# Kernel optimization log

Hardware: AMD Instinct MI355X
Metric: run time of the kernel (lower is better)

Reference implementation:

```python
import jax, jax.numpy as jnp
import numpy as np

H, NH, R = 128, 8, 6
NB = 2                  # geometric interaction blocks
BS, L, K = 16, 64, 16   # graphs, blocks/graph, atoms/block
NBLK = BS * L           # 1024 blocks total
N = NBLK * K            # 16384 atoms
E = 262144              # atom-level edges
EB = 512                # block-level edges per graph
CUTOFF = 8.0


def _mha(x, in_w, in_b, out_w, out_b):
    # torch nn.MultiheadAttention (batch_first, eval / no dropout). x: [B,S,H]
    B_, S, _ = x.shape
    qkv = x @ in_w + in_b                     # [B,S,3H]
    q, k, v = jnp.split(qkv, 3, axis=-1)
    dh = H // NH
    q = q.reshape(B_, S, NH, dh)
    k = k.reshape(B_, S, NH, dh)
    v = v.reshape(B_, S, NH, dh)
    scores = jnp.einsum('bind,bjnd->bnij', q, k) / np.sqrt(dh).astype(np.float32)
    attn = jax.nn.softmax(scores, axis=-1)
    o = jnp.einsum('bnij,bjnd->bind', attn, v).reshape(B_, S, H)
    return o @ out_w + out_b


def _forward(A, atom_positions, B_types, coords, edge_index, block_edges,
             emb_atom, emb_pos, emb_block, rbf_freq,
             inter_w1, inter_b1, inter_w2, inter_b2,
             upd_w1, upd_b1, upd_w2, upd_b2,
             edge_w1, edge_b1, edge_w2, edge_b2,
             attn_in_w, attn_in_b, attn_out_w, attn_out_b,
             ln_g, ln_b, fin_w1, fin_b1, fin_w2, fin_b2, fin_w3, fin_b3):
    block_id = jnp.repeat(jnp.arange(NBLK), K)  # uniform K atoms per block
    # atom embedding + position embedding + broadcast block embedding
    x = emb_atom[A] + emb_pos[atom_positions] + emb_block[B_types][block_id]  # [N,H]

    # ---- GeometricAtomProcessor ----
    i, j = edge_index[0], edge_index[1]
    d = jnp.linalg.norm(coords[i] - coords[j], axis=-1)       # [E]
    u = jnp.clip(d / CUTOFF, 1e-3, None)
    # DimeNet envelope, exponent=5 -> p=6: 1/u + a u^5 + b u^6 + c u^7
    env = 1.0 / u - 28.0 * u**5 + 48.0 * u**6 - 21.0 * u**7
    rbf = env[:, None] * jnp.sin(rbf_freq[None, :] * u[:, None])  # [E,R]

    for b in range(NB):
        ef = jnp.concatenate([x[i], x[j], rbf], axis=-1)       # [E,2H+R] gather
        m = jax.nn.silu(ef @ inter_w1[b] + inter_b1[b]) @ inter_w2[b] + inter_b2[b]
        agg = jax.ops.segment_sum(m, i, num_segments=N)        # index_add_ scatter
        ui = jnp.concatenate([x, agg], axis=-1)
        x = jax.nn.silu(ui @ upd_w1[b] + upd_b1[b]) @ upd_w2[b] + upd_b2[b] + x

    # scatter_mean over block_id (uniform blocks -> reshape mean)
    blocks = x.reshape(NBLK, K, H).mean(axis=1).reshape(BS, L, H)

    # ---- per-graph block-edge attention (batched over graphs) ----
    src, dst = block_edges[..., 0], block_edges[..., 1]        # [BS,EB]
    bidx = jnp.arange(BS)[:, None]
    ef = jnp.concatenate([blocks[bidx, src], blocks[bidx, dst]], axis=-1)  # [BS,EB,2H]
    ef = jax.nn.relu(ef @ edge_w1 + edge_b1) @ edge_w2 + edge_b2
    ea = _mha(ef, attn_in_w, attn_in_b, attn_out_w, attn_out_b)            # [BS,EB,H]
    seg = (src + bidx * L).reshape(-1)
    sums = jax.ops.segment_sum(ea.reshape(-1, H), seg, num_segments=NBLK)
    cnt = jax.ops.segment_sum(jnp.ones((BS * EB,), ea.dtype), seg, num_segments=NBLK)
    blocks = blocks + (sums / jnp.maximum(cnt, 1.0)[:, None]).reshape(BS, L, H)

    # ---- block self-attention + mean pool ----
    att = _mha(blocks, attn_in_w, attn_in_b, attn_out_w, attn_out_b)
    g = att.mean(axis=1)                                       # [BS,H]
    mu = g.mean(-1, keepdims=True)
    var = ((g - mu) ** 2).mean(-1, keepdims=True)
    g = (g - mu) / jnp.sqrt(var + 1e-5) * ln_g + ln_b
    h1 = jax.nn.relu(g @ fin_w1 + fin_b1)
    h2 = jax.nn.relu(h1 @ fin_w2 + fin_b2)
    return (h2 @ fin_w3 + fin_b3).squeeze(-1)                  # [BS]


def setup_inputs() -> dict:
    key = jax.random.key(0)
    ks = jax.random.split(key, 40)
    def nrm(k, shape, s=0.05):
        return jax.random.normal(k, shape, jnp.float32) * s
    inp = {}
    inp['A'] = jax.random.randint(ks[0], (N,), 0, 100)
    inp['atom_positions'] = jax.random.randint(ks[1], (N,), 0, 16)
    inp['B_types'] = jax.random.randint(ks[2], (NBLK,), 0, 1000)
    inp['coords'] = jax.random.uniform(ks[3], (N, 3), jnp.float32, 0.0, 20.0)
    inp['edge_index'] = jax.random.randint(ks[4], (2, E), 0, N)
    inp['block_edges'] = jax.random.randint(ks[5], (BS, EB, 2), 0, L)
    inp['emb_atom'] = nrm(ks[6], (100, H), 0.5)
    inp['emb_pos'] = nrm(ks[7], (16, H), 0.5)
    inp['emb_block'] = nrm(ks[8], (1000, H), 0.5)
    inp['rbf_freq'] = (jnp.arange(1, R + 1, dtype=jnp.float32) * np.pi)
    inp['inter_w1'] = nrm(ks[9], (NB, 2 * H + R, H))
    inp['inter_b1'] = jnp.zeros((NB, H), jnp.float32)
    inp['inter_w2'] = nrm(ks[10], (NB, H, H))
    inp['inter_b2'] = jnp.zeros((NB, H), jnp.float32)
    inp['upd_w1'] = nrm(ks[11], (NB, 2 * H, H))
    inp['upd_b1'] = jnp.zeros((NB, H), jnp.float32)
    inp['upd_w2'] = nrm(ks[12], (NB, H, H))
    inp['upd_b2'] = jnp.zeros((NB, H), jnp.float32)
    inp['edge_w1'] = nrm(ks[13], (2 * H, H))
    inp['edge_b1'] = jnp.zeros((H,), jnp.float32)
    inp['edge_w2'] = nrm(ks[14], (H, H))
    inp['edge_b2'] = jnp.zeros((H,), jnp.float32)
    inp['attn_in_w'] = nrm(ks[15], (H, 3 * H))
    inp['attn_in_b'] = jnp.zeros((3 * H,), jnp.float32)
    inp['attn_out_w'] = nrm(ks[16], (H, H))
    inp['attn_out_b'] = jnp.zeros((H,), jnp.float32)
    inp['ln_g'] = jnp.ones((H,), jnp.float32)
    inp['ln_b'] = jnp.zeros((H,), jnp.float32)
    inp['fin_w1'] = nrm(ks[17], (H, H))
    inp['fin_b1'] = jnp.zeros((H,), jnp.float32)
    inp['fin_w2'] = nrm(ks[18], (H, H))
    inp['fin_b2'] = jnp.zeros((H,), jnp.float32)
    inp['fin_w3'] = nrm(ks[19], (H, 1))
    inp['fin_b3'] = jnp.zeros((1,), jnp.float32)
    return inp


def reference(A, atom_positions, B_types, coords, edge_index, block_edges,
              emb_atom, emb_pos, emb_block, rbf_freq,
              inter_w1, inter_b1, inter_w2, inter_b2,
              upd_w1, upd_b1, upd_w2, upd_b2,
              edge_w1, edge_b1, edge_w2, edge_b2,
              attn_in_w, attn_in_b, attn_out_w, attn_out_b,
              ln_g, ln_b, fin_w1, fin_b1, fin_w2, fin_b2, fin_w3, fin_b3):
    return _forward(A, atom_positions, B_types, coords, edge_index, block_edges,
                    emb_atom, emb_pos, emb_block, rbf_freq,
                    inter_w1, inter_b1, inter_w2, inter_b2,
                    upd_w1, upd_b1, upd_w2, upd_b2,
                    edge_w1, edge_b1, edge_w2, edge_b2,
                    attn_in_w, attn_in_b, attn_out_w, attn_out_b,
                    ln_g, ln_b, fin_w1, fin_b1, fin_w2, fin_b2, fin_w3, fin_b3)
```

## Files before the change

### kernel.cpp

```cpp
#include <hip/hip_runtime.h>
#include <math.h>

#define H 128
#define NHD 8
#define DH 16
#define RB 6
#define NBI 2
#define BSG 16
#define LBLK 64
#define KATOM 16
#define NBLKT 1024
#define NA 16384
#define NE 262144
#define EBE 512

__device__ __forceinline__ float fsilu(float v) {
  return v * __builtin_amdgcn_rcpf(1.0f + __expf(-v));
}

typedef short v4s __attribute__((ext_vector_type(4)));
typedef float f32x4 __attribute__((ext_vector_type(4)));

__device__ __forceinline__ short f2bf(float f) {
  union { float f; unsigned u; } v; v.f = f;
  unsigned r = v.u + 0x7fffu + ((v.u >> 16) & 1u);
  return (short)(r >> 16);
}

__device__ __forceinline__ float bf2f(short s) {
  union { unsigned u; float f; } v;
  v.u = ((unsigned)(unsigned short)s) << 16;
  return v.f;
}

#if defined(__has_builtin)
#if __has_builtin(__builtin_amdgcn_mfma_f32_16x16x16bf16_1k)
#define HAVE_MFMA16_1K 1
#endif
#endif

#ifdef HAVE_MFMA16_1K
__device__ __forceinline__ f32x4 mfma16(v4s a, v4s b, f32x4 c) {
  return __builtin_amdgcn_mfma_f32_16x16x16bf16_1k(a, b, c, 0, 0, 0);
}
#else
typedef short v8s __attribute__((ext_vector_type(8)));
__device__ __forceinline__ f32x4 mfma16(v4s a, v4s b, f32x4 c) {
  v8s a8 = {a[0], a[1], a[2], a[3], 0, 0, 0, 0};
  v8s b8 = {b[0], b[1], b[2], b[3], 0, 0, 0, 0};
  return __builtin_amdgcn_mfma_f32_16x16x32_bf16(a8, b8, c, 0, 0, 0);
}
#endif

__global__ __launch_bounds__(256) void k_hist(
    const int* __restrict__ ei, int* __restrict__ cnt)
{
  int e = blockIdx.x * 256 + threadIdx.x;
  atomicAdd(&cnt[ei[e]], 1);
}

__global__ __launch_bounds__(1024) void k_scan(
    const int* __restrict__ cnt, int* __restrict__ off,
    int* __restrict__ cur, float* __restrict__ cntf)
{
  __shared__ int ps[1024];
  int t = threadIdx.x;
  int base = t * 16;
  int local[16];
  int s = 0;
  #pragma unroll
  for (int k = 0; k < 16; ++k) { local[k] = s; s += cnt[base + k]; }
  ps[t] = s;
  __syncthreads();
  for (int d = 1; d < 1024; d <<= 1) {
    int v = (t >= d) ? ps[t - d] : 0;
    __syncthreads();
    ps[t] += v;
    __syncthreads();
  }
  int offset = (t == 0) ? 0 : ps[t - 1];
  #pragma unroll
  for (int k = 0; k < 16; ++k) {
    int o = offset + local[k];
    off[base + k] = o;
    cur[base + k] = o;
    cntf[base + k] = (float)cnt[base + k];
  }
  if (t == 1023) off[NA] = offset + s;
}

__global__ __launch_bounds__(256) void k_scatter_b(
    const int* __restrict__ ei, const int* __restrict__ ej,
    const float* __restrict__ coords, const float* __restrict__ freq,
    int* __restrict__ cur, int* __restrict__ ej_s, float* __restrict__ rbf_s,
    const int* __restrict__ bedges, int* __restrict__ blist,
    int* __restrict__ boff, float* __restrict__ ind)
{
  __shared__ int hist[64], offs[65], curs[64];
  int t = threadIdx.x;
  if (blockIdx.x < NE / 256) {
    int e = blockIdx.x * 256 + t;
    int i = ei[e], j = ej[e];
    int pos = atomicAdd(&cur[i], 1);
    ej_s[pos] = j;
    float dx = coords[i*3+0] - coords[j*3+0];
    float dy = coords[i*3+1] - coords[j*3+1];
    float dz = coords[i*3+2] - coords[j*3+2];
    float d = sqrtf(dx*dx + dy*dy + dz*dz);
    float u = fmaxf(d * 0.125f, 1e-3f);
    float u2 = u*u, u4 = u2*u2, u5 = u4*u, u6 = u5*u, u7 = u6*u;
    float env = 1.0f/u - 28.0f*u5 + 48.0f*u6 - 21.0f*u7;
    #pragma unroll
    for (int r = 0; r < RB; ++r)
      rbf_s[(size_t)pos*RB + r] = env * __sinf(freq[r] * u);
    return;
  }
  int b = blockIdx.x - NE / 256;
  if (t < 64) hist[t] = 0;
  __syncthreads();
  for (int e = t; e < EBE; e += 256) atomicAdd(&hist[bedges[(b*EBE + e)*2]], 1);
  __syncthreads();
  if (t == 0) {
    offs[0] = 0;
    for (int k = 0; k < 64; ++k) offs[k+1] = offs[k] + hist[k];
  }
  __syncthreads();
  if (t < 64) curs[t] = offs[t];
  __syncthreads();
  for (int e = t; e < EBE; e += 256) {
    int src = bedges[(b*EBE + e)*2];
    int pos = atomicAdd(&curs[src], 1);
    blist[b*EBE + pos] = e;
  }
  if (t < 65) boff[b*65 + t] = offs[t];
  if (t < 64) ind[b*64 + t] = (hist[t] > 0) ? 1.0f : 0.0f;
}

__global__ __launch_bounds__(256) void k_prep(
    const float* __restrict__ W2base, const float* __restrict__ U1base,
    const float* __restrict__ b2base, float* __restrict__ bvecbase,
    short* __restrict__ wt_u1base,
    const float* __restrict__ inter_w1, const float* __restrict__ upd_w2,
    const float* __restrict__ edge_w1, const float* __restrict__ edge_w2,
    const float* __restrict__ attn_in_w,
    short* __restrict__ wt_pq, short* __restrict__ wt_u2,
    short* __restrict__ wt_e1, short* __restrict__ wt_e2,
    short* __restrict__ wt_in)
{
  int bx = blockIdx.x, tid = threadIdx.x;
  if (bx < 128) {
    int k = bx, y = tid >> 7, c = tid & 127;
    const float* W2 = W2base + (size_t)y * H * H;
    const float* U1 = U1base + (size_t)y * 2 * H * H;
    const float* b2 = b2base + y * H;
    float* bvec = bvecbase + y * H;
    short* wt1 = wt_u1base + (size_t)y * 128 * 256;
    const float* U1b = U1 + 128 * H;
    wt1[c * 256 + k] = f2bf(U1[k * H + c]);
    float s = 0.0f;
    for (int t = 0; t < H; ++t) s += W2[k * H + t] * U1b[t * H + c];
    wt1[c * 256 + 128 + k] = f2bf(s);
    if (k == 0) {
      float sb = 0.0f;
      for (int t = 0; t < H; ++t) sb += b2[t] * U1b[t * H + c];
      bvec[c] = sb;
    }
    return;
  }
  int idx = (bx - 128) * 256 + tid;
  {
    int k = idx & 127, col = (idx >> 7) & 127, y = (idx >> 14) & 1, b = idx >> 15;
// ... 134 lines not shown
      v4s a = *(const v4s*)&As[rowb + c][kc*64 + ks*16 + g*4];
      #pragma unroll
      for (int ct = 0; ct < 8; ++ct) {
        v4s bf = *(const v4s*)&Ws[ct*16 + c][ks*16 + g*4];
        acc[ct] = mfma16(a, bf, acc[ct]);
      }
    }
  }
  #pragma unroll
  for (int ct = 0; ct < 8; ++ct) {
    int col = ct*16 + c;
    float bb = y ? 0.0f : b1[col];
    #pragma unroll
    for (int r = 0; r < 4; ++r) {
      int row = m0 + rowb + g*4 + r;
      C[(size_t)row*H + col] = f2bf(acc[ct][r] + bb);
    }
  }
}

__global__ __launch_bounds__(256) void k_pq_mfma(
    const float* __restrict__ x, const short* __restrict__ WtPQ,
    const float* __restrict__ b1,
    short* __restrict__ P, short* __restrict__ Q)
{
  __shared__ short As[64][136];
  __shared__ short Ws[128][72];
  int tid = threadIdx.x;
  int m0 = blockIdx.x * 64;
  int y = blockIdx.y;
  const short* Wt = WtPQ + (size_t)y * 128 * 128;
  short* C = y ? Q : P;
  for (int idx = tid; idx < 64*32; idx += 256) {
    int r = idx >> 5, c4 = idx & 31;
    float4 v = *(const float4*)&x[(size_t)(m0 + r)*H + c4*4];
    short4 s4 = { f2bf(v.x), f2bf(v.y), f2bf(v.z), f2bf(v.w) };
    *(short4*)&As[r][c4*4] = s4;
  }
  int lane = tid & 63, wv = tid >> 6;
  int c = lane & 15, g = lane >> 4;
  int rowb = wv * 16;
  f32x4 acc[8];
  #pragma unroll
  for (int t = 0; t < 8; ++t) acc[t] = (f32x4){0,0,0,0};
  for (int kc = 0; kc < 2; ++kc) {
    __syncthreads();
    {
      int col = tid >> 1, hh = (tid & 1) * 32;
      const int4* src = (const int4*)&Wt[col*128 + kc*64 + hh];
      int4 a0 = src[0], a1 = src[1], a2 = src[2], a3 = src[3];
      *(int4*)&Ws[col][hh] = a0;      *(int4*)&Ws[col][hh+8] = a1;
      *(int4*)&Ws[col][hh+16] = a2;   *(int4*)&Ws[col][hh+24] = a3;
    }
    __syncthreads();
    #pragma unroll
    for (int ks = 0; ks < 4; ++ks) {
      v4s a = *(const v4s*)&As[rowb + c][kc*64 + ks*16 + g*4];
      #pragma unroll
      for (int ct = 0; ct < 8; ++ct) {
        v4s bf = *(const v4s*)&Ws[ct*16 + c][ks*16 + g*4];
        acc[ct] = mfma16(a, bf, acc[ct]);
      }
    }
  }
  #pragma unroll
  for (int ct = 0; ct < 8; ++ct) {
    int col = ct*16 + c;
    float bb = y ? 0.0f : b1[col];
    #pragma unroll
    for (int r = 0; r < 4; ++r) {
      int row = m0 + rowb + g*4 + r;
      C[(size_t)row*H + col] = f2bf(acc[ct][r] + bb);
    }
  }
}

__global__ __launch_bounds__(256) void k_upd_mfma(
    const float* __restrict__ x, const float* __restrict__ Hagg,
    const short* __restrict__ Wt1,
    const float* __restrict__ b1, const float* __restrict__ bvec,
    const float* __restrict__ cntf,
    const short* __restrict__ Wt2,
    const float* __restrict__ b2,
    float* __restrict__ xout, float* __restrict__ blocksOut)
{
  __shared__ short As[64][264];
  __shared__ short Ws[128][72];
  __shared__ short Us[64][136];
  int tid = threadIdx.x;
  int m0 = blockIdx.x * 64;
  for (int idx = tid; idx < 64*64; idx += 256) {
    int r = idx >> 6, c4 = idx & 63;
    const float* src = (c4 < 32) ? &x[(size_t)(m0 + r)*H + c4*4]
                                 : &Hagg[(size_t)(m0 + r)*H + (c4-32)*4];
    float4 v = *(const float4*)src;
    short4 s4 = { f2bf(v.x), f2bf(v.y), f2bf(v.z), f2bf(v.w) };
    *(short4*)&As[r][c4*4] = s4;
  }
  int lane = tid & 63, wv = tid >> 6;
  int c = lane & 15, g = lane >> 4;
  int rowb = wv * 16;
  f32x4 acc[8];
  #pragma unroll
  for (int t = 0; t < 8; ++t) acc[t] = (f32x4){0,0,0,0};
  for (int kc = 0; kc < 4; ++kc) {
    __syncthreads();
    {
      int col = tid >> 1, hh = (tid & 1) * 32;
      const int4* src = (const int4*)&Wt1[col*256 + kc*64 + hh];
      int4 a0 = src[0], a1 = src[1], a2 = src[2], a3 = src[3];
      *(int4*)&Ws[col][hh] = a0;      *(int4*)&Ws[col][hh+8] = a1;
      *(int4*)&Ws[col][hh+16] = a2;   *(int4*)&Ws[col][hh+24] = a3;
    }
    __syncthreads();
    #pragma unroll
    for (int ks = 0; ks < 4; ++ks) {
      v4s a = *(const v4s*)&As[rowb + c][kc*64 + ks*16 + g*4];
      #pragma unroll
      for (int ct = 0; ct < 8; ++ct) {
        v4s bf = *(const v4s*)&Ws[ct*16 + c][ks*16 + g*4];
        acc[ct] = mfma16(a, bf, acc[ct]);
      }
    }
  }
  {
    float cr[4];
    #pragma unroll
    for (int r = 0; r < 4; ++r) cr[r] = cntf[m0 + rowb + g*4 + r];
    #pragma unroll
    for (int ct = 0; ct < 8; ++ct) {
      int col = ct*16 + c;
      float bb = b1[col], bv = bvec[col];
      #pragma unroll
      for (int r = 0; r < 4; ++r) {
        float v = acc[ct][r] + bb + bv * cr[r];
        Us[rowb + g*4 + r][col] = f2bf(fsilu(v));
        acc[ct][r] = 0.0f;
      }
    }
  }
  for (int kc = 0; kc < 2; ++kc) {
    __syncthreads();
    {
      int col = tid >> 1, hh = (tid & 1) * 32;
      const int4* src = (const int4*)&Wt2[col*128 + kc*64 + hh];
      int4 a0 = src[0], a1 = src[1], a2 = src[2], a3 = src[3];
      *(int4*)&Ws[col][hh] = a0;      *(int4*)&Ws[col][hh+8] = a1;
      *(int4*)&Ws[col][hh+16] = a2;   *(int4*)&Ws[col][hh+24] = a3;
    }
    __syncthreads();
    #pragma unroll
    for (int ks = 0; ks < 4; ++ks) {
      v4s a = *(const v4s*)&Us[rowb + c][kc*64 + ks*16 + g*4];
      #pragma unroll
      for (int ct = 0; ct < 8; ++ct) {
        v4s bf = *(const v4s*)&Ws[ct*16 + c][ks*16 + g*4];
        acc[ct] = mfma16(a, bf, acc[ct]);
      }
    }
  }
  #pragma unroll
  for (int ct = 0; ct < 8; ++ct) {
    int col = ct*16 + c;
    float bb = b2[col];
    float bs = 0.0f;
    #pragma unroll
    for (int r = 0; r < 4; ++r) {
      int row = m0 + rowb + g*4 + r;
      float v = acc[ct][r] + bb + x[(size_t)row*H + col];
      xout[(size_t)row*H + col] = v;
      bs += v;
    }
    if (blocksOut) {
      bs += __shfl_xor(bs, 16);
      bs += __shfl_xor(bs, 32);
      if (g == 0)
        blocksOut[(size_t)(m0/KATOM + wv)*H + col] = bs * (1.0f / KATOM);
    }
  }
}

__global__ __launch_bounds__(256) void k_eprep_mfma(
    const short* __restrict__ Pb, const short* __restrict__ Qb,
    const int* __restrict__ bedges,
    const short* __restrict__ Wt2e, const float* __restrict__ b2e,
    const short* __restrict__ WtIn, const float* __restrict__ bin,
    float* __restrict__ qkv)
{
  __shared__ short As[64][136];
  __shared__ short Ws[128][72];
  __shared__ short Us[64][136];
  int tid = threadIdx.x;
  int m0 = blockIdx.x * 64;
  for (int idx = tid; idx < 64*32; idx += 256) {
    int r = idx >> 5, c4 = idx & 31;
    int row = m0 + r;
    int g = row >> 9;
    int src = bedges[row*2], dst = bedges[row*2 + 1];
    short4 p4 = *(const short4*)&Pb[(size_t)(g*LBLK + src)*H + c4*4];
    short4 q4 = *(const short4*)&Qb[(size_t)(g*LBLK + dst)*H + c4*4];
    short4 s4;
    s4.x = f2bf(fmaxf(bf2f(p4.x) + bf2f(q4.x), 0.0f));
    s4.y = f2bf(fmaxf(bf2f(p4.y) + bf2f(q4.y), 0.0f));
    s4.z = f2bf(fmaxf(bf2f(p4.z) + bf2f(q4.z), 0.0f));
    s4.w = f2bf(fmaxf(bf2f(p4.w) + bf2f(q4.w), 0.0f));
    *(short4*)&As[r][c4*4] = s4;
  }
  int lane = tid & 63, wv = tid >> 6;
  int c = lane & 15, g = lane >> 4;
  int rowb = wv * 16;
  f32x4 acc[8];
  #pragma unroll
  for (int t = 0; t < 8; ++t) acc[t] = (f32x4){0,0,0,0};
  for (int kc = 0; kc < 2; ++kc) {
    __syncthreads();
    {
      int col = tid >> 1, hh = (tid & 1) * 32;
      const int4* src = (const int4*)&Wt2e[col*128 + kc*64 + hh];
      int4 a0 = src[0], a1 = src[1], a2 = src[2], a3 = src[3];
      *(int4*)&Ws[col][hh] = a0;      *(int4*)&Ws[col][hh+8] = a1;
      *(int4*)&Ws[col][hh+16] = a2;   *(int4*)&Ws[col][hh+24] = a3;
    }
    __syncthreads();
    #pragma unroll
    for (int ks = 0; ks < 4; ++ks) {
      v4s a = *(const v4s*)&As[rowb + c][kc*64 + ks*16 + g*4];
      #pragma unroll
      for (int ct = 0; ct < 8; ++ct) {
        v4s bf = *(const v4s*)&Ws[ct*16 + c][ks*16 + g*4];
        acc[ct] = mfma16(a, bf, acc[ct]);
      }
    }
  }
  #pragma unroll
  for (int ct = 0; ct < 8; ++ct) {
    int col = ct*16 + c;
    float bb = b2e[col];
    #pragma unroll
    for (int r = 0; r < 4; ++r) {
      Us[rowb + g*4 + r][col] = f2bf(acc[ct][r] + bb);
      acc[ct][r] = 0.0f;
    }
  }
  for (int cc = 0; cc < 3; ++cc) {
    for (int kc = 0; kc < 2; ++kc) {
      __syncthreads();
      {
        int col = tid >> 1, hh = (tid & 1) * 32;
        const int4* src = (const int4*)&WtIn[(size_t)(cc*128 + col)*128 + kc*64 + hh];
        int4 a0 = src[0], a1 = src[1], a2 = src[2], a3 = src[3];
        *(int4*)&Ws[col][hh] = a0;      *(int4*)&Ws[col][hh+8] = a1;
        *(int4*)&Ws[col][hh+16] = a2;   *(int4*)&Ws[col][hh+24] = a3;
      }
      __syncthreads();
      #pragma unroll
      for (int ks = 0; ks < 4; ++ks) {
        v4s a = *(const v4s*)&Us[rowb + c][kc*64 + ks*16 + g*4];
        #pragma unroll
        for (int ct = 0; ct < 8; ++ct) {
          v4s bf = *(const v4s*)&Ws[ct*16 + c][ks*16 + g*4];
          acc[ct] = mfma16(a, bf, acc[ct]);
        }
      }
    }
    #pragma unroll
    for (int ct = 0; ct < 8; ++ct) {
      int col = ct*16 + c;
      float bb = bin[cc*128 + col];
      #pragma unroll
      for (int r = 0; r < 4; ++r) {
        int row = m0 + rowb + g*4 + r;
        qkv[(size_t)row*384 + cc*128 + col] = acc[ct][r] + bb;
        acc[ct][r] = 0.0f;
      }
    }
  }
}

__global__ __launch_bounds__(256) void k_bprep(
    const float* __restrict__ bsum, const float* __restrict__ Wout,
    const float* __restrict__ bout, const float* __restrict__ ind,
    const float* __restrict__ blocks,
    const float* __restrict__ Win, const float* __restrict__ bin,
    float* __restrict__ qkv)
{
  __shared__ float As[32][128];
  __shared__ float Ws[16][128];
  __shared__ float Us[32][128];
  int tid = threadIdx.x;
  int m0 = blockIdx.x * 32;
  int chunk = blockIdx.y;
  for (int idx = tid; idx < 32*32; idx += 256) {
    int r = idx >> 5, k4 = idx & 31;
    *(float4*)&As[r][k4*4] = *(const float4*)&bsum[(size_t)(m0 + r)*H + k4*4];
  }
  int rr = tid >> 5;
  int cq = tid & 31;
  float acc[4][4] = {};
  for (int kk0 = 0; kk0 < 128; kk0 += 16) {
    __syncthreads();
    for (int idx = tid; idx < 16*32; idx += 256) {
      int kr = idx >> 5, c4 = idx & 31;
      *(float4*)&Ws[kr][c4*4] = *(const float4*)&Wout[(size_t)(kk0 + kr)*H + c4*4];
    }
    __syncthreads();
    #pragma unroll
    for (int k4 = 0; k4 < 4; ++k4) {
      float4 w0 = *(const float4*)&Ws[k4*4+0][cq*4];
      float4 w1 = *(const float4*)&Ws[k4*4+1][cq*4];
      float4 w2 = *(const float4*)&Ws[k4*4+2][cq*4];
      float4 w3 = *(const float4*)&Ws[k4*4+3][cq*4];
      #pragma unroll
      for (int i = 0; i < 4; ++i) {
        float4 a = *(const float4*)&As[rr + 8*i][kk0 + k4*4];
        acc[i][0] += a.x*w0.x + a.y*w1.x + a.z*w2.x + a.w*w3.x;
        acc[i][1] += a.x*w0.y + a.y*w1.y + a.z*w2.y + a.w*w3.y;
        acc[i][2] += a.x*w0.z + a.y*w1.z + a.z*w2.z + a.w*w3.z;
        acc[i][3] += a.x*w0.w + a.y*w1.w + a.z*w2.w + a.w*w3.w;
      }
    }
  }
  #pragma unroll
  for (int i = 0; i < 4; ++i) {
    int m = m0 + rr + 8*i;
    float bs = ind[m];
    float4 u;
    float* pu = &u.x;
    #pragma unroll
    for (int j = 0; j < 4; ++j) {
      int c = cq*4 + j;
      pu[j] = acc[i][j] + bout[c] * bs + blocks[(size_t)m*H + c];
    }
    *(float4*)&Us[rr + 8*i][cq*4] = u;
    acc[i][0] = 0.0f; acc[i][1] = 0.0f; acc[i][2] = 0.0f; acc[i][3] = 0.0f;
  }
  for (int kk0 = 0; kk0 < 128; kk0 += 16) {
    __syncthreads();
    for (int idx = tid; idx < 16*32; idx += 256) {
      int kr = idx >> 5, c4 = idx & 31;
      *(float4*)&Ws[kr][c4*4] =
          *(const float4*)&Win[(size_t)(kk0 + kr)*384 + chunk*128 + c4*4];
    }
    __syncthreads();
    #pragma unroll
    for (int k4 = 0; k4 < 4; ++k4) {
      float4 w0 = *(const float4*)&Ws[k4*4+0][cq*4];
      float4 w1 = *(const float4*)&Ws[k4*4+1][cq*4];
      float4 w2 = *(const float4*)&Ws[k4*4+2][cq*4];
      float4 w3 = *(const float4*)&Ws[k4*4+3][cq*4];
      #pragma unroll
      for (int i = 0; i < 4; ++i) {
        float4 a = *(const float4*)&Us[rr + 8*i][kk0 + k4*4];
        acc[i][0] += a.x*w0.x + a.y*w1.x + a.z*w2.x + a.w*w3.x;
        acc[i][1] += a.x*w0.y + a.y*w1.y + a.z*w2.y + a.w*w3.y;
        acc[i][2] += a.x*w0.z + a.y*w1.z + a.z*w2.z + a.w*w3.z;
        acc[i][3] += a.x*w0.w + a.y*w1.w + a.z*w2.w + a.w*w3.w;
      }
    }
  }
  #pragma unroll
  for (int i = 0; i < 4; ++i) {
    int m = m0 + rr + 8*i;
    float4 out;
    float* po = &out.x;
    #pragma unroll
    for (int j = 0; j < 4; ++j)
      po[j] = acc[i][j] + bin[chunk*128 + cq*4 + j];
    *(float4*)&qkv[(size_t)m*384 + chunk*128 + cq*4] = out;
  }
}

__global__ __launch_bounds__(256) void k_eattn(
    const float* __restrict__ qkv, float* __restrict__ ea)
{
  constexpr int S = EBE;
  constexpr int NR = BSG * NHD * S;
  __shared__ short Ks[S * DH];
  __shared__ short Vt[DH * (S + 4)];
  int rb = blockIdx.x & 3;
  int bh = blockIdx.x >> 2;
  int b = bh >> 3, h = bh & 7;
  const float* base = qkv + (size_t)b * S * 384;
  int tid = threadIdx.x;
  for (int t = tid; t < S * 4; t += 256) {
    int j = t >> 2, q4 = t & 3;
    float4 kv = *(const float4*)(base + (size_t)j * 384 + 128 + h * DH + q4 * 4);
    float4 vv = *(const float4*)(base + (size_t)j * 384 + 256 + h * DH + q4 * 4);
    short* kp = &Ks[j * DH + q4 * 4];
    kp[0] = f2bf(kv.x); kp[1] = f2bf(kv.y); kp[2] = f2bf(kv.z); kp[3] = f2bf(kv.w);
    Vt[(q4*4 + 0) * (S + 4) + j] = f2bf(vv.x);
    Vt[(q4*4 + 1) * (S + 4) + j] = f2bf(vv.y);
    Vt[(q4*4 + 2) * (S + 4) + j] = f2bf(vv.z);
    Vt[(q4*4 + 3) * (S + 4) + j] = f2bf(vv.w);
  }
  __syncthreads();
  int lane = tid & 63, wv = tid >> 6;
  int q = lane & 15;
  int g = lane >> 4;
  for (int qs = 0; qs < 2; ++qs) {
    int row = rb * 128 + qs * 64 + wv * 16 + q;
    float4 qv = *(const float4*)(base + (size_t)row * 384 + h * DH + g * 4);
    v4s qf = { f2bf(qv.x), f2bf(qv.y), f2bf(qv.z), f2bf(qv.w) };
    f32x4 zero = {0.f, 0.f, 0.f, 0.f};
    f32x4 o = zero;
    float m = -1e30f, lsum = 0.0f;
    for (int t = 0; t < S / 16; ++t) {
      v4s ak = *(const v4s*)&Ks[(t * 16 + q) * DH + g * 4];
      f32x4 st = mfma16(ak, qf, zero);
      float tm = fmaxf(fmaxf(st[0], st[1]), fmaxf(st[2], st[3]));
      tm = fmaxf(tm, __shfl_xor(tm, 16));
      tm = fmaxf(tm, __shfl_xor(tm, 32));
      float mn = fmaxf(m, tm);
      float corr = __expf((m - mn) * 0.25f);
      m = mn;
      float p0 = __expf((st[0] - mn) * 0.25f);
      float p1 = __expf((st[1] - mn) * 0.25f);
      float p2 = __expf((st[2] - mn) * 0.25f);
      float p3 = __expf((st[3] - mn) * 0.25f);
      lsum = lsum * corr + ((p0 + p1) + (p2 + p3));
      o[0] *= corr; o[1] *= corr; o[2] *= corr; o[3] *= corr;
      v4s pb = { f2bf(p0), f2bf(p1), f2bf(p2), f2bf(p3) };
      v4s av = *(const v4s*)&Vt[q * (S + 4) + t * 16 + g * 4];
      o = mfma16(av, pb, o);
    }
    float lt = lsum + __shfl_xor(lsum, 16);
    lt += __shfl_xor(lt, 32);
    float inv = 1.0f / lt;
    float4 outv = { o[0]*inv, o[1]*inv, o[2]*inv, o[3]*inv };
    ((float4*)ea)[(size_t)g * NR + (size_t)bh * S + row] = outv;
  }
}

__global__ __launch_bounds__(256) void k_bsum_gather(
    const float* __restrict__ ea, const int* __restrict__ blist,
    const int* __restrict__ boff, float* __restrict__ bsum)
{
  constexpr int NR = BSG * NHD * EBE;
  int idx = blockIdx.x * 256 + threadIdx.x;
  int i = idx >> 5, c4 = idx & 31;
  int b = i >> 6, blk = i & 63;
  int h = c4 >> 2, d4 = c4 & 3;
  int e0 = boff[b*65 + blk], e1 = boff[b*65 + blk + 1];
  const float4* ea4 = (const float4*)ea;
  size_t basein = (size_t)d4 * NR + (size_t)(b*NHD + h) * EBE;
  float4 s = {0, 0, 0, 0};
  for (int e = e0; e < e1; ++e) {
    int srow = blist[b*EBE + e];
    float4 v = ea4[basein + srow];
    s.x += v.x; s.y += v.y; s.z += v.z; s.w += v.w;
  }
  float cnt = (float)(e1 - e0);
  float sc = (cnt > 0.0f) ? (1.0f / cnt) : 0.0f;
  float4 o = {s.x*sc, s.y*sc, s.z*sc, s.w*sc};
  *(float4*)&bsum[(size_t)i*H + c4*4] = o;
}

__global__ __launch_bounds__(256) void k_attnS(
    const float* __restrict__ qkv, float* __restrict__ m2)
{
  __shared__ float Ks[4][LBLK][DH];
  __shared__ float Vs[4][LBLK][DH];
  __shared__ float red[4][LBLK][DH + 1];
  int b = blockIdx.x >> 1, hq = blockIdx.x & 1;
  int tid = threadIdx.x;
  const float* base = qkv + (size_t)b * LBLK * 384;
  for (int t = tid; t < 1024; t += 256) {
    int hl = t >> 8, j = (t >> 2) & 63, d4 = t & 3;
    int h = hq*4 + hl;
    *(float4*)&Ks[hl][j][d4*4] = *(const float4*)(base + (size_t)j*384 + 128 + h*DH + d4*4);
    *(float4*)&Vs[hl][j][d4*4] = *(const float4*)(base + (size_t)j*384 + 256 + h*DH + d4*4);
  }
  __syncthreads();
  int hl = tid >> 6, s = tid & 63;
  int h = hq*4 + hl;
  const float4* qp = (const float4*)(base + (size_t)s * 384 + h * DH);
  float4 q0 = qp[0], q1 = qp[1], q2 = qp[2], q3 = qp[3];
  float m = -1e30f, l = 0.0f;
  float4 o0 = {0,0,0,0}, o1 = {0,0,0,0}, o2 = {0,0,0,0}, o3 = {0,0,0,0};
  for (int c0 = 0; c0 < LBLK; c0 += 32) {
    float scv[32];
    float mc = -1e30f;
    #pragma unroll
    for (int j = 0; j < 32; ++j) {
      float4 k0 = *(const float4*)&Ks[hl][c0+j][0];
      float4 k1 = *(const float4*)&Ks[hl][c0+j][4];
// ... 58 lines not shown
__global__ __launch_bounds__(128) void k_final(
    const float* __restrict__ m2, const float* __restrict__ out_w,
    const float* __restrict__ out_b, const float* __restrict__ lng,
    const float* __restrict__ lnb, const float* __restrict__ w1,
    const float* __restrict__ b1, const float* __restrict__ w2,
    const float* __restrict__ b2, const float* __restrict__ w3,
    const float* __restrict__ b3, float* __restrict__ out)
{
  __shared__ float buf[128];
  __shared__ float red[128];
  int b = blockIdx.x, t = threadIdx.x;
  buf[t] = m2[b*H + t];
  __syncthreads();
  float g = out_b[t];
  for (int k = 0; k < H; ++k) g += buf[k] * out_w[k*H + t];
  float mu = bsum128(g, red) * (1.0f / H);
  float df = g - mu;
  float var = bsum128(df * df, red) * (1.0f / H);
  float gn = df / sqrtf(var + 1e-5f) * lng[t] + lnb[t];
  __syncthreads();
  buf[t] = gn; __syncthreads();
  float h1 = b1[t];
  for (int k = 0; k < H; ++k) h1 += buf[k] * w1[k*H + t];
  h1 = fmaxf(h1, 0.0f);
  __syncthreads();
  buf[t] = h1; __syncthreads();
  float h2 = b2[t];
  for (int k = 0; k < H; ++k) h2 += buf[k] * w2[k*H + t];
  h2 = fmaxf(h2, 0.0f);
  float tot = bsum128(h2 * w3[t], red);
  if (t == 0) out[b] = tot + b3[0];
}

extern "C" void kernel_launch(void* const* d_in, const int* in_sizes, int n_in,
                              void* d_out, int out_size, void* d_ws, size_t ws_size,
                              hipStream_t stream) {
  (void)in_sizes; (void)n_in; (void)out_size; (void)ws_size;
  const int*   A          = (const int*)d_in[0];
  const int*   apos       = (const int*)d_in[1];
  const int*   btypes     = (const int*)d_in[2];
  const float* coords     = (const float*)d_in[3];
  const int*   edge_index = (const int*)d_in[4];
  const int*   bedges     = (const int*)d_in[5];
  const float* emb_atom   = (const float*)d_in[6];
  const float* emb_pos    = (const float*)d_in[7];
  const float* emb_block  = (const float*)d_in[8];
  const float* rbf_freq   = (const float*)d_in[9];
  const float* inter_w1   = (const float*)d_in[10];
  const float* inter_b1   = (const float*)d_in[11];
  const float* inter_w2   = (const float*)d_in[12];
  const float* inter_b2   = (const float*)d_in[13];
  const float* upd_w1     = (const float*)d_in[14];
  const float* upd_b1     = (const float*)d_in[15];
  const float* upd_w2     = (const float*)d_in[16];
  const float* upd_b2     = (const float*)d_in[17];
  const float* edge_w1    = (const float*)d_in[18];
  const float* edge_b1    = (const float*)d_in[19];
  const float* edge_w2    = (const float*)d_in[20];
  const float* edge_b2    = (const float*)d_in[21];
  const float* attn_in_w  = (const float*)d_in[22];
  const float* attn_in_b  = (const float*)d_in[23];
  const float* attn_out_w = (const float*)d_in[24];
  const float* attn_out_b = (const float*)d_in[25];
  const float* ln_g       = (const float*)d_in[26];
  const float* ln_b       = (const float*)d_in[27];
  const float* fin_w1     = (const float*)d_in[28];
  const float* fin_b1     = (const float*)d_in[29];
  const float* fin_w2     = (const float*)d_in[30];
  const float* fin_b2     = (const float*)d_in[31];
  const float* fin_w3     = (const float*)d_in[32];
  const float* fin_b3     = (const float*)d_in[33];
  float* out = (float*)d_out;

  float* ws = (float*)d_ws;
  float* x      = ws + 0;
  short* P      = (short*)(ws + 2097152);
  short* Q      = (short*)(ws + 4194304);
  float* Hagg   = ws + 6291456;
  float* rbf_s  = ws + 8388608;
  float* cntf   = ws + 9961472;
  float* blocks = ws + 9977856;
  short* Pb     = (short*)(ws + 10108928);
  short* Qb     = (short*)(ws + 10240000);
  float* qkv    = ws + 12468224;
  float* bsum   = ws + 15613952;
  float* ind    = ws + 15746048;
  float* m2     = ws + 15747072;
  int* blist    = (int*)(ws + 15749120);
  int* boff     = (int*)(ws + 15757312);
  int* ej_s   = (int*)(ws + 10371072);
  int* off    = (int*)(ws + 10371072 + 262144);
  int* cur    = (int*)(ws + 10371072 + 278784);
  int* cnt    = (int*)(ws + 10371072 + 295168);
  float* bvec = ws + 10371072 + 311552;
  short* wt_pq = (short*)(ws + 16777216);
  short* wt_u1 = (short*)(ws + 16777216 + 32768);
  short* wt_u2 = (short*)(ws + 16777216 + 65536);
  short* wt_e1 = (short*)(ws + 16777216 + 81920);
  short* wt_e2 = (short*)(ws + 16777216 + 98304);
  short* wt_in = (short*)(ws + 16777216 + 106496);
  float* ea     = ws + 10371072;

  const int* ei = edge_index;
  const int* ej = edge_index + NE;

  (void)hipMemsetAsync(cnt, 0, NA * sizeof(int), stream);
  k_hist<<<NE/256, 256, 0, stream>>>(ei, cnt);
  k_scan<<<1, 1024, 0, stream>>>(cnt, off, cur, cntf);
  k_scatter_b<<<NE/256 + BSG, 256, 0, stream>>>(ei, ej, coords, rbf_freq, cur,
                                                ej_s, rbf_s,
                                                bedges, blist, boff, ind);
  k_prep<<<384, 256, 0, stream>>>(inter_w2, upd_w1, inter_b2, bvec, wt_u1,
                                  inter_w1, upd_w2, edge_w1, edge_w2, attn_in_w,
                                  wt_pq, wt_u2, wt_e1, wt_e2, wt_in);

  for (int b = 0; b < NBI; ++b) {
    if (b == 0) {
      k_embed_pq<<<dim3(NA/64, 2), 256, 0, stream>>>(
          A, apos, btypes, emb_atom, emb_pos, emb_block,
          wt_pq, inter_b1, x, P, Q);
    } else {
      k_pq_mfma<<<dim3(NA/64, 2), 256, 0, stream>>>(
          x, wt_pq + (size_t)b*2*128*128, inter_b1 + b*H, P, Q);
    }
    const float* w1 = inter_w1 + (size_t)b * 262 * H;
    k_edge_csr<<<NA/4, 256, 0, stream>>>(P, Q, rbf_s, w1 + 256*H, ej_s, off, Hagg);
    k_upd_mfma<<<NA/64, 256, 0, stream>>>(
        x, Hagg, wt_u1 + (size_t)b*128*256, upd_b1 + b*H, bvec + b*H, cntf,
        wt_u2 + (size_t)b*128*128, upd_b2 + b*H, x,
        (b == NBI-1) ? blocks : nullptr);
  }

  k_pq_mfma<<<dim3(NBLKT/64, 2), 256, 0, stream>>>(blocks, wt_e1, edge_b1, Pb, Qb);
  k_eprep_mfma<<<BSG*EBE/64, 256, 0, stream>>>(Pb, Qb, bedges, wt_e2, edge_b2,
                                               wt_in, attn_in_b, qkv);
  k_eattn<<<BSG*NHD*(EBE/128), 256, 0, stream>>>(qkv, ea);
  k_bsum_gather<<<NBLKT*32/256, 256, 0, stream>>>(ea, blist, boff, bsum);
  k_bprep<<<dim3(NBLKT/32, 3), 256, 0, stream>>>(bsum, attn_out_w, attn_out_b, ind,
                                                 blocks, attn_in_w, attn_in_b, qkv);
  k_attnS<<<BSG*2, 256, 0, stream>>>(qkv, m2);
  k_final<<<BSG, 128, 0, stream>>>(m2, attn_out_w, attn_out_b, ln_g, ln_b,
                                   fin_w1, fin_b1, fin_w2, fin_b2, fin_w3, fin_b3, out);
}
```

Baseline: 400.5 us.

## Fuse next-layer PQ projection into update kernel and store attention QKV in bf16 head-major layout

Several independent changes. The second-layer P/Q projection now runs inside the first update kernel, reusing the freshly written x tile in shared memory, which removes one launch and a reload of x. The edge-attention Q/K/V are written as bf16 in a per-head contiguous layout, so the attention kernel copies K straight into shared memory instead of converting strided fp32. k_bprep no longer splits its three output chunks across a grid dimension; one block computes all three and so repeats the first GEMM only once, at the cost of a third of the grid. The single-block scan now uses wave shuffles instead of a shared-memory Hillis-Steele loop.

Measured after the change: 410.2 us. 2.4% more time.

```diff
diff --git a/kernel.cpp b/kernel.cpp
--- a/kernel.cpp
+++ b/kernel.cpp
@@ -63,30 +63,45 @@
     const int* __restrict__ cnt, int* __restrict__ off,
     int* __restrict__ cur, float* __restrict__ cntf)
 {
-  __shared__ int ps[1024];
+  __shared__ int wsum[16];
   int t = threadIdx.x;
+  int lane = t & 63, wid = t >> 6;
   int base = t * 16;
   int local[16];
   int s = 0;
   #pragma unroll
-  for (int k = 0; k < 16; ++k) { local[k] = s; s += cnt[base + k]; }
-  ps[t] = s;
-  __syncthreads();
-  for (int d = 1; d < 1024; d <<= 1) {
-    int v = (t >= d) ? ps[t - d] : 0;
-    __syncthreads();
-    ps[t] += v;
-    __syncthreads();
-  }
-  int offset = (t == 0) ? 0 : ps[t - 1];
+  for (int k = 0; k < 16; ++k) {
+    local[k] = s;
+    int c = cnt[base + k];
+    cntf[base + k] = (float)c;
+    s += c;
+  }
+  int tot = s;
+  #pragma unroll
+  for (int d = 1; d < 64; d <<= 1) {
+    int v = __shfl_up(s, d);
+    if (lane >= d) s += v;
+  }
+  if (lane == 63) wsum[wid] = s;
+  __syncthreads();
+  if (t < 16) {
+    int w = wsum[t];
+    #pragma unroll
+    for (int d = 1; d < 16; d <<= 1) {
+      int v = __shfl_up(w, d, 16);
+      if (t >= d) w += v;
+    }
+    wsum[t] = w;
+  }
+  __syncthreads();
+  int offset = (wid ? wsum[wid - 1] : 0) + (s - tot);
   #pragma unroll
   for (int k = 0; k < 16; ++k) {
     int o = offset + local[k];
     off[base + k] = o;
     cur[base + k] = o;
-    cntf[base + k] = (float)cnt[base + k];
-  }
-  if (t == 1023) off[NA] = offset + s;
+  }
+  if (t == 1023) off[NA] = wsum[15];
 }
 
 __global__ __launch_bounds__(256) void k_scatter_b(
@@ -387,7 +402,10 @@
     const float* __restrict__ cntf,
     const short* __restrict__ Wt2,
     const float* __restrict__ b2,
-    float* __restrict__ xout, float* __restrict__ blocksOut)
+    float* __restrict__ xout, float* __restrict__ blocksOut,
+    const short* __restrict__ WtN,
+    const float* __restrict__ b1N,
+    short* __restrict__ Pn, short* __restrict__ Qn)
 {
   __shared__ short As[64][264];
   __shared__ short Ws[128][72];
@@ -474,6 +492,7 @@
       int row = m0 + rowb + g*4 + r;
       float v = acc[ct][r] + bb + x[(size_t)row*H + col];
       xout[(size_t)row*H + col] = v;
+      if (WtN) As[rowb + g*4 + r][col] = f2bf(v);
       bs += v;
     }
     if (blocksOut) {
@@ -483,6 +502,45 @@
         blocksOut[(size_t)(m0/KATOM + wv)*H + col] = bs * (1.0f / KATOM);
     }
   }
+  if (WtN) {
+    __syncthreads();
+    for (int y = 0; y < 2; ++y) {
+      const short* Wt = WtN + (size_t)y * 128 * 128;
+      #pragma unroll
+      for (int t2 = 0; t2 < 8; ++t2) acc[t2] = (f32x4){0,0,0,0};
+      for (int kc = 0; kc < 2; ++kc) {
+        __syncthreads();
+        {
+          int col = tid >> 1, hh = (tid & 1) * 32;
+          const int4* src = (const int4*)&Wt[col*128 + kc*64 + hh];
+          int4 a0 = src[0], a1 = src[1], a2 = src[2], a3 = src[3];
+          *(int4*)&Ws[col][hh] = a0;      *(int4*)&Ws[col][hh+8] = a1;
+          *(int4*)&Ws[col][hh+16] = a2;   *(int4*)&Ws[col][hh+24] = a3;
+        }
+        __syncthreads();
+        #pragma unroll
+        for (int ks = 0; ks < 4; ++ks) {
+          v4s a = *(const v4s*)&As[rowb + c][kc*64 + ks*16 + g*4];
+          #pragma unroll
+          for (int ct = 0; ct < 8; ++ct) {
+            v4s bf = *(const v4s*)&Ws[ct*16 + c][ks*16 + g*4];
+            acc[ct] = mfma16(a, bf, acc[ct]);
+          }
+        }
+      }
+      short* C = y ? Qn : Pn;
+      #pragma unroll
+      for (int ct = 0; ct < 8; ++ct) {
+        int col = ct*16 + c;
+        float bb = y ? 0.0f : b1N[col];
+        #pragma unroll
+        for (int r = 0; r < 4; ++r) {
+          int row = m0 + rowb + g*4 + r;
+          C[(size_t)row*H + col] = f2bf(acc[ct][r] + bb);
+        }
+      }
+    }
+  }
 }
 
 __global__ __launch_bounds__(256) void k_eprep_mfma(
@@ -490,7 +548,7 @@
     const int* __restrict__ bedges,
     const short* __restrict__ Wt2e, const float* __restrict__ b2e,
     const short* __restrict__ WtIn, const float* __restrict__ bin,
-    float* __restrict__ qkv)
+    short* __restrict__ Qe, short* __restrict__ Ke, short* __restrict__ Ve)
 {
   __shared__ short As[64][136];
   __shared__ short Ws[128][72];
@@ -575,7 +633,14 @@
       #pragma unroll
       for (int r = 0; r < 4; ++r) {
         int row = m0 + rowb + g*4 + r;
-        qkv[(size_t)row*384 + cc*128 + col] = acc[ct][r] + bb;
+        short val = f2bf(acc[ct][r] + bb);
+        if (cc == 0) {
+          Qe[(size_t)row*H + col] = val;
+        } else {
+          size_t o = (((size_t)((row >> 9) * NHD + (col >> 4))) * EBE
+                      + (row & 511)) * DH + (col & 15);
+          ((cc == 1) ? Ke : Ve)[o] = val;
+        }
         acc[ct][r] = 0.0f;
       }
     }
@@ -594,7 +659,6 @@
   __shared__ float Us[32][128];
   int tid = threadIdx.x;
   int m0 = blockIdx.x * 32;
-  int chunk = blockIdx.y;
   for (int idx = tid; idx < 32*32; idx += 256) {
     int r = idx >> 5, k4 = idx & 31;
     *(float4*)&As[r][k4*4] = *(const float4*)&bsum[(size_t)(m0 + r)*H + k4*4];
@@ -639,44 +703,49 @@
     *(float4*)&Us[rr + 8*i][cq*4] = u;
     acc[i][0] = 0.0f; acc[i][1] = 0.0f; acc[i][2] = 0.0f; acc[i][3] = 0.0f;
   }
-  for (int kk0 = 0; kk0 < 128; kk0 += 16) {
-    __syncthreads();
-    for (int idx = tid; idx < 16*32; idx += 256) {
-      int kr = idx >> 5, c4 = idx & 31;
-      *(float4*)&Ws[kr][c4*4] =
-          *(const float4*)&Win[(size_t)(kk0 + kr)*384 + chunk*128 + c4*4];
-    }
-    __syncthreads();
-    #pragma unroll
-    for (int k4 = 0; k4 < 4; ++k4) {
-      float4 w0 = *(const float4*)&Ws[k4*4+0][cq*4];
-      float4 w1 = *(const float4*)&Ws[k4*4+1][cq*4];
-      float4 w2 = *(const float4*)&Ws[k4*4+2][cq*4];
-      float4 w3 = *(const float4*)&Ws[k4*4+3][cq*4];
-      #pragma unroll
-      for (int i = 0; i < 4; ++i) {
-        float4 a = *(const float4*)&Us[rr + 8*i][kk0 + k4*4];
-        acc[i][0] += a.x*w0.x + a.y*w1.x + a.z*w2.x + a.w*w3.x;
-        acc[i][1] += a.x*w0.y + a.y*w1.y + a.z*w2.y + a.w*w3.y;
-        acc[i][2] += a.x*w0.z + a.y*w1.z + a.z*w2.z + a.w*w3.z;
-        acc[i][3] += a.x*w0.w + a.y*w1.w + a.z*w2.w + a.w*w3.w;
-      }
-    }
-  }
-  #pragma unroll
-  for (int i = 0; i < 4; ++i) {
-    int m = m0 + rr + 8*i;
-    float4 out;
-    float* po = &out.x;
-    #pragma unroll
-    for (int j = 0; j < 4; ++j)
-      po[j] = acc[i][j] + bin[chunk*128 + cq*4 + j];
-    *(float4*)&qkv[(size_t)m*384 + chunk*128 + cq*4] = out;
+  for (int cc = 0; cc < 3; ++cc) {
+    for (int kk0 = 0; kk0 < 128; kk0 += 16) {
+      __syncthreads();
+      for (int idx = tid; idx < 16*32; idx += 256) {
+        int kr = idx >> 5, c4 = idx & 31;
+        *(float4*)&Ws[kr][c4*4] =
+            *(const float4*)&Win[(size_t)(kk0 + kr)*384 + cc*128 + c4*4];
+      }
+      __syncthreads();
+      #pragma unroll
+      for (int k4 = 0; k4 < 4; ++k4) {
+        float4 w0 = *(const float4*)&Ws[k4*4+0][cq*4];
+        float4 w1 = *(const float4*)&Ws[k4*4+1][cq*4];
+        float4 w2 = *(const float4*)&Ws[k4*4+2][cq*4];
+        float4 w3 = *(const float4*)&Ws[k4*4+3][cq*4];
+        #pragma unroll
+        for (int i = 0; i < 4; ++i) {
+          float4 a = *(const float4*)&Us[rr + 8*i][kk0 + k4*4];
+          acc[i][0] += a.x*w0.x + a.y*w1.x + a.z*w2.x + a.w*w3.x;
+          acc[i][1] += a.x*w0.y + a.y*w1.y + a.z*w2.y + a.w*w3.y;
+          acc[i][2] += a.x*w0.z + a.y*w1.z + a.z*w2.z + a.w*w3.z;
+          acc[i][3] += a.x*w0.w + a.y*w1.w + a.z*w2.w + a.w*w3.w;
+        }
+      }
+    }
+    #pragma unroll
+    for (int i = 0; i < 4; ++i) {
+      int m = m0 + rr + 8*i;
+      float4 out;
+      float* po = &out.x;
+      #pragma unroll
+      for (int j = 0; j < 4; ++j) {
+        po[j] = acc[i][j] + bin[cc*128 + cq*4 + j];
+        acc[i][j] = 0.0f;
+      }
+      *(float4*)&qkv[(size_t)m*384 + cc*128 + cq*4] = out;
+    }
   }
 }
 
 __global__ __launch_bounds__(256) void k_eattn(
-    const float* __restrict__ qkv, float* __restrict__ ea)
+    const short* __restrict__ Qe, const short* __restrict__ Ke,
+    const short* __restrict__ Ve, float* __restrict__ ea)
 {
   constexpr int S = EBE;
   constexpr int NR = BSG * NHD * S;
@@ -685,18 +754,18 @@
   int rb = blockIdx.x & 3;
   int bh = blockIdx.x >> 2;
   int b = bh >> 3, h = bh & 7;
-  const float* base = qkv + (size_t)b * S * 384;
   int tid = threadIdx.x;
-  for (int t = tid; t < S * 4; t += 256) {
-    int j = t >> 2, q4 = t & 3;
-    float4 kv = *(const float4*)(base + (size_t)j * 384 + 128 + h * DH + q4 * 4);
-    float4 vv = *(const float4*)(base + (size_t)j * 384 + 256 + h * DH + q4 * 4);
-    short* kp = &Ks[j * DH + q4 * 4];
-    kp[0] = f2bf(kv.x); kp[1] = f2bf(kv.y); kp[2] = f2bf(kv.z); kp[3] = f2bf(kv.w);
-    Vt[(q4*4 + 0) * (S + 4) + j] = f2bf(vv.x);
-    Vt[(q4*4 + 1) * (S + 4) + j] = f2bf(vv.y);
-    Vt[(q4*4 + 2) * (S + 4) + j] = f2bf(vv.z);
-    Vt[(q4*4 + 3) * (S + 4) + j] = f2bf(vv.w);
+  const short* kb = Ke + (size_t)bh * S * DH;
+  const short* vb = Ve + (size_t)bh * S * DH;
+  for (int t = tid; t < S * DH / 8; t += 256)
+    ((int4*)Ks)[t] = ((const int4*)kb)[t];
+  for (int t = tid; t < S * 2; t += 256) {
+    int j = t >> 1, half = t & 1;
+    int4 v8 = ((const int4*)vb)[t];
+    short vs[8]; *(int4*)vs = v8;
+    #pragma unroll
+    for (int k = 0; k < 8; ++k)
+      Vt[(half*8 + k) * (S + 4) + j] = vs[k];
   }
   __syncthreads();
   int lane = tid & 63, wv = tid >> 6;
@@ -704,8 +773,7 @@
   int g = lane >> 4;
   for (int qs = 0; qs < 2; ++qs) {
     int row = rb * 128 + qs * 64 + wv * 16 + q;
-    float4 qv = *(const float4*)(base + (size_t)row * 384 + h * DH + g * 4);
-    v4s qf = { f2bf(qv.x), f2bf(qv.y), f2bf(qv.z), f2bf(qv.w) };
+    v4s qf = *(const v4s*)&Qe[((size_t)b * S + row) * H + h * DH + g * 4];
     f32x4 zero = {0.f, 0.f, 0.f, 0.f};
     f32x4 o = zero;
     float m = -1e30f, lsum = 0.0f;
@@ -930,7 +998,10 @@
   float* blocks = ws + 9977856;
   short* Pb     = (short*)(ws + 10108928);
   short* Qb     = (short*)(ws + 10240000);
-  float* qkv    = ws + 12468224;
+  short* Qe     = (short*)(ws + 12468224);
+  short* Ke     = (short*)(ws + 12468224 + 524288);
+  short* Ve     = (short*)(ws + 12468224 + 1048576);
+  float* qkvB   = ws + 12468224 + 1572864;
   float* bsum   = ws + 15613952;
   float* ind    = ws + 15746048;
   float* m2     = ws + 15747072;
@@ -962,31 +1033,31 @@
                                   inter_w1, upd_w2, edge_w1, edge_w2, attn_in_w,
                                   wt_pq, wt_u2, wt_e1, wt_e2, wt_in);
 
-  for (int b = 0; b < NBI; ++b) {
-    if (b == 0) {
-      k_embed_pq<<<dim3(NA/64, 2), 256, 0, stream>>>(
-          A, apos, btypes, emb_atom, emb_pos, emb_block,
-          wt_pq, inter_b1, x, P, Q);
-    } else {
-      k_pq_mfma<<<dim3(NA/64, 2), 256, 0, stream>>>(
-          x, wt_pq + (size_t)b*2*128*128, inter_b1 + b*H, P, Q);
-    }
-    const float* w1 = inter_w1 + (size_t)b * 262 * H;
-    k_edge_csr<<<NA/4, 256, 0, stream>>>(P, Q, rbf_s, w1 + 256*H, ej_s, off, Hagg);
-    k_upd_mfma<<<NA/64, 256, 0, stream>>>(
-        x, Hagg, wt_u1 + (size_t)b*128*256, upd_b1 + b*H, bvec + b*H, cntf,
-        wt_u2 + (size_t)b*128*128, upd_b2 + b*H, x,
-        (b == NBI-1) ? blocks : nullptr);
-  }
+  k_embed_pq<<<dim3(NA/64, 2), 256, 0, stream>>>(
+      A, apos, btypes, emb_atom, emb_pos, emb_block,
+      wt_pq, inter_b1, x, P, Q);
+  k_edge_csr<<<NA/4, 256, 0, stream>>>(P, Q, rbf_s,
+                                       inter_w1 + 256*H, ej_s, off, Hagg);
+  k_upd_mfma<<<NA/64, 256, 0, stream>>>(
+      x, Hagg, wt_u1, upd_b1, bvec, cntf, wt_u2, upd_b2, x, nullptr,
+      wt_pq + (size_t)1*2*128*128, inter_b1 + H, P, Q);
+
+  k_edge_csr<<<NA/4, 256, 0, stream>>>(P, Q, rbf_s,
+                                       inter_w1 + (size_t)262*H + 256*H,
+                                       ej_s, off, Hagg);
+  k_upd_mfma<<<NA/64, 256, 0, stream>>>(
+      x, Hagg, wt_u1 + (size_t)128*256, upd_b1 + H, bvec + H, cntf,
+      wt_u2 + (size_t)128*128, upd_b2 + H, x, blocks,
+      nullptr, nullptr, nullptr, nullptr);
 
   k_pq_mfma<<<dim3(NBLKT/64, 2), 256, 0, stream>>>(blocks, wt_e1, edge_b1, Pb, Qb);
   k_eprep_mfma<<<BSG*EBE/64, 256, 0, stream>>>(Pb, Qb, bedges, wt_e2, edge_b2,
-                                               wt_in, attn_in_b, qkv);
-  k_eattn<<<BSG*NHD*(EBE/128), 256, 0, stream>>>(qkv, ea);
+                                               wt_in, attn_in_b, Qe, Ke, Ve);
+  k_eattn<<<BSG*NHD*(EBE/128), 256, 0, stream>>>(Qe, Ke, Ve, ea);
   k_bsum_gather<<<NBLKT*32/256, 256, 0, stream>>>(ea, blist, boff, bsum);
-  k_bprep<<<dim3(NBLKT/32, 3), 256, 0, stream>>>(bsum, attn_out_w, attn_out_b, ind,
-                                                 blocks, attn_in_w, attn_in_b, qkv);
-  k_attnS<<<BSG*2, 256, 0, stream>>>(qkv, m2);
+  k_bprep<<<NBLKT/32, 256, 0, stream>>>(bsum, attn_out_w, attn_out_b, ind,
+                                        blocks, attn_in_w, attn_in_b, qkvB);
+  k_attnS<<<BSG*2, 256, 0, stream>>>(qkvB, m2);
   k_final<<<BSG, 128, 0, stream>>>(m2, attn_out_w, attn_out_b, ln_g, ln_b,
                                    fin_w1, fin_b1, fin_w2, fin_b2, fin_w3, fin_b3, out);
 }
```
